# Optimization experiments

Measured on AMD Instinct MI355X. Metric: run time of the kernel, lower is better.

## Reference

```python
import jax, jax.numpy as jnp
import numpy as np

B, S, H = 4, 2048, 512
DEPTH, EXP = 2, 4
MAX_LR = 0.1
C = 8            # n_chunks
L = S // C       # chunk length
HE = H * EXP


def _l2norm(x, eps=1e-12):
    n = jnp.sqrt(jnp.sum(x * x, axis=-1, keepdims=True))
    return x / jnp.maximum(n, eps)


def _mem_fwd(mw1, mb1, mw2, mb2, x):
    # ResLinear: residual MLP blocks, x <- x + W2 @ silu(W1 @ x + b1) + b2
    for d in range(DEPTH):
        h = jax.nn.silu(x @ mw1[d].T + mb1[d])
        x = x + h @ mw2[d].T + mb2[d]
    return x


def setup_inputs() -> dict:
    key = jax.random.key(0)
    ks = jax.random.split(key, 9)
    s = 1.0 / np.sqrt(H)
    s2 = 1.0 / np.sqrt(HE)
    return {
        "x": jax.random.normal(ks[0], (B, S, H), jnp.float32),
        "wq": jax.random.normal(ks[1], (H, H), jnp.float32) * s, "bq": jnp.zeros((H,), jnp.float32),
        "wk": jax.random.normal(ks[2], (H, H), jnp.float32) * s, "bk": jnp.zeros((H,), jnp.float32),
        "wv": jax.random.normal(ks[3], (H, H), jnp.float32) * s, "bv": jnp.zeros((H,), jnp.float32),
        "wlr": jax.random.normal(ks[4], (1, H), jnp.float32) * s, "blr": jnp.zeros((1,), jnp.float32),
        "wf": jax.random.normal(ks[5], (1, H), jnp.float32) * s, "bf": jnp.zeros((1,), jnp.float32),
        "wm": jax.random.normal(ks[6], (1, H), jnp.float32) * s, "bm": jnp.zeros((1,), jnp.float32),
        "mw1": jax.random.normal(ks[7], (DEPTH, HE, H), jnp.float32) * s,
        "mb1": jnp.zeros((DEPTH, HE), jnp.float32),
        "mw2": jax.random.normal(ks[8], (DEPTH, H, HE), jnp.float32) * s2,
        "mb2": jnp.zeros((DEPTH, H), jnp.float32),
        "mom_w1": jnp.zeros((DEPTH, HE, H), jnp.float32),
        "mom_b1": jnp.zeros((DEPTH, HE), jnp.float32),
        "mom_w2": jnp.zeros((DEPTH, H, HE), jnp.float32),
        "mom_b2": jnp.zeros((DEPTH, H), jnp.float32),
    }


def reference(x, wq, bq, wk, bk, wv, bv, wlr, blr, wf, bf, wm, bm,
              mw1, mb1, mw2, mb2, mom_w1, mom_b1, mom_w2, mom_b2):
    # projections (non-generating path; S % C == 0 so no padding)
    q = _l2norm(x @ wq.T + bq)                            # [B,S,H]
    k = _l2norm(x @ wk.T + bk).reshape(B, C, L, H)
    v = (x @ wv.T + bv).reshape(B, C, L, H)
    lr = jax.nn.sigmoid(x @ wlr.T + blr).reshape(B, C, L, 1) * MAX_LR
    forget = jax.nn.sigmoid(x @ wf.T + bf).reshape(B, C, L, 1)
    momg = jax.nn.sigmoid(x @ wm.T + bm).reshape(B, C, L, 1)

    mem = (mw1, mb1, mw2, mb2)

    def chunk_loss(mem_params, k_c, v_c, lr_c):
        # k_c,v_c: [B,L,H]; lr_c: [B,L,1]
        preds = _mem_fwd(*mem_params, k_c)
        loss = jnp.mean((preds - v_c) ** 2, axis=-1)      # [B,L]
        return jnp.sum(loss * lr_c[..., 0])

    # per-chunk synthetic gradients of the memory MLP, then mean over chunks
    grads = jax.vmap(jax.grad(chunk_loss), in_axes=(None, 1, 1, 1))(mem, k, v, lr)
    grads = jax.tree_util.tree_map(lambda g: jnp.mean(g, axis=0), grads)

    alpha = jnp.mean(forget, axis=(1, 2, 3))              # [B] forget gate
    theta = jnp.mean(lr, axis=(1, 2, 3))                  # [B] adaptive lr
    eta = jnp.mean(momg, axis=(1, 2, 3))                  # [B] momentum gate

    def update(p, g, m):
        shp = (B,) + (1,) * p.ndim
        a, t, e = alpha.reshape(shp), theta.reshape(shp), eta.reshape(shp)
        m_b = e * m[None] - t * g[None]                   # [B,*p.shape]
        return jnp.mean(p[None] * (1.0 - a) + m_b, axis=0)

    moms = (mom_w1, mom_b1, mom_w2, mom_b2)
    new_mem = tuple(update(p, g, m) for p, g, m in zip(mem, grads, moms))

    return _mem_fwd(*new_mem, q)                          # [B,S,H]
```

## Files before the change

### kernel.cpp

```cpp
#include <hip/hip_runtime.h>
#include <cstdint>
#include <cstddef>


#define NROWS 8192
#define HDIM  512
#define HEDIM 2048
#define NCHUNK 8
#define BK    64
#define DPCOEF (2.0f / (HDIM * NCHUNK))

typedef unsigned short u16;
typedef __attribute__((ext_vector_type(8))) unsigned short u16x8;
typedef __attribute__((ext_vector_type(8))) short bf16x8;
typedef __attribute__((ext_vector_type(4))) float f32x4;

__device__ __forceinline__ float sigmoidf_(float x){ return 1.0f/(1.0f+__expf(-x)); }
__device__ __forceinline__ float siluf_(float x){ return x*sigmoidf_(x); }
__device__ __forceinline__ float dsiluf_(float x){ float s=sigmoidf_(x); return s*(1.0f+x*(1.0f-s)); }
__device__ __forceinline__ u16 bf1_(float x){
    union{float f; unsigned u;} v; v.f = x;
    return (u16)((v.u + 0x7fffu + ((v.u>>16)&1u)) >> 16);
}
__device__ __forceinline__ unsigned bfpack_(float a, float b){
    union{float f; unsigned u;} ua, ub; ua.f = a; ub.f = b;
    unsigned ra = (ua.u + 0x7fffu + ((ua.u>>16)&1u)) >> 16;
    unsigned rb = (ub.u + 0x7fffu + ((ub.u>>16)&1u)) & 0xffff0000u;
    return ra | rb;
}
__device__ __forceinline__ float bf2f_(u16 h){
    union{unsigned u; float f;} v; v.u = ((unsigned)h) << 16; return v.f;
}
__device__ __forceinline__ int swkey_(int row){
    return (((row>>3)&1)<<2) | (((row>>4)&1)<<1) | ((row>>5)&1);
}
__device__ __forceinline__ void gl_lds16(const u16* g, u16* l){
    __builtin_amdgcn_global_load_lds(
        (const __attribute__((address_space(1))) unsigned*)g,
        (__attribute__((address_space(3))) unsigned*)l, 16, 0, 0);
}
__device__ __forceinline__ void bar_(){ asm volatile("s_barrier" ::: "memory"); }
#define VMCNT8  asm volatile("s_waitcnt vmcnt(8)" ::: "memory")
#define VMCNT0  asm volatile("s_waitcnt vmcnt(0)" ::: "memory")
#define LGKM0   asm volatile("s_waitcnt lgkmcnt(0)" ::: "memory")

template<int MODE, bool ATR>
__global__ __launch_bounds__(256)
void mgemm_k(const u16* __restrict__ A, const u16* __restrict__ B,
             const float* __restrict__ bias, const float* __restrict__ resF,
             const u16* __restrict__ resB, const u16* __restrict__ aux,
             const float* __restrict__ vf, const float* __restrict__ lrs,
             float* __restrict__ outF, u16* __restrict__ outB, u16* __restrict__ outB2,
             int M, int N, int K, int lda, int ldb, int ldv)
{
    constexpr int NBUF = ATR ? 1 : 2;
    __shared__ __align__(128) u16 As[NBUF][128*64];
    __shared__ __align__(128) u16 Bs[NBUF][128*64];
    const int tid = threadIdx.x;
    const int lane = tid & 63, wvi = tid >> 6;
    const int wm = wvi >> 1, wn = wvi & 1;
    const int lr = lane & 15, lq = lane >> 4;

    const int gx = gridDim.x;
    const int nwg = gx * gridDim.y;
    int bid = blockIdx.y * gx + blockIdx.x;
    bid = (bid & 7) * (nwg >> 3) + (bid >> 3);
    const int m0 = (bid / gx) * 128, n0 = (bid % gx) * 128;

    int kbeg = 0, kend = K;
    if (MODE == 3){ const int ks = K >> 4; kbeg = blockIdx.z * ks; kend = kbeg + ks; }
    const int nk = (kend - kbeg) / BK;

    f32x4 acc[4][4];
    const f32x4 zz = {0.f,0.f,0.f,0.f};
    #pragma unroll
    for (int i = 0; i < 4; ++i)
        #pragma unroll
        for (int j = 0; j < 4; ++j) acc[i][j] = zz;

    const int mc = tid & 15, kp = tid >> 4;
    const int tkey = (((mc&1)<<2)|(((mc>>1)&1)<<1)|((mc>>2)&1));
    const int tcs = ((kp >> 1) ^ tkey) * 8 + (kp & 1) * 4;
    u16x8 rgA0, rgA1, rgA2, rgA3, rgB0, rgB1, rgB2, rgB3;

    auto stageNT = [&](int k0, int b){
        #pragma unroll
        for (int it = 0; it < 4; ++it){
            const int seg = it*4 + wvi;
            const int key = (((seg&1)<<2)|(((seg>>1)&1)<<1)|((seg>>2)&1));
            const int row = seg*8 + (lane>>3);
            const int chunk = (lane&7) ^ key;
            gl_lds16(A + (size_t)(m0+row)*lda + k0 + chunk*8, &As[b][seg*512]);
            gl_lds16(B + (size_t)(n0+row)*ldb + k0 + chunk*8, &Bs[b][seg*512]);
        }
    };
    auto gloadTN = [&](int k0){
        const u16* pa = A + (size_t)(k0 + 4*kp) * lda + m0 + mc*8;
        rgA0 = *(const u16x8*)pa;          rgA1 = *(const u16x8*)(pa + lda);
        rgA2 = *(const u16x8*)(pa+2*lda);  rgA3 = *(const u16x8*)(pa + 3*lda);
        const u16* pb = B + (size_t)(k0 + 4*kp) * ldb + n0 + mc*8;
        rgB0 = *(const u16x8*)pb;          rgB1 = *(const u16x8*)(pb + ldb);
        rgB2 = *(const u16x8*)(pb+2*ldb);  rgB3 = *(const u16x8*)(pb + 3*ldb);
    };
    auto dswriteTN = [&](){
        #pragma unroll
        for (int j = 0; j < 8; ++j){
            uint2 w;
            w.x = (unsigned)rgA0[j] | ((unsigned)rgA1[j] << 16);
            w.y = (unsigned)rgA2[j] | ((unsigned)rgA3[j] << 16);
            *(uint2*)&As[0][(mc*8 + j)*64 + tcs] = w;
            uint2 v;
            v.x = (unsigned)rgB0[j] | ((unsigned)rgB1[j] << 16);
            v.y = (unsigned)rgB2[j] | ((unsigned)rgB3[j] << 16);
            *(uint2*)&Bs[0][(mc*8 + j)*64 + tcs] = v;
        }
    };
    auto mfmaStep = [&](int b){
        #pragma unroll
        for (int ks = 0; ks < 2; ++ks) {
            bf16x8 afr[4], bfr[4];
            #pragma unroll
            for (int i = 0; i < 4; ++i){
                const int ra = wm*64 + i*16 + lr, rb = wn*64 + i*16 + lr;
                afr[i] = *(const bf16x8*)&As[b][ra*64 + (((ks*4 + lq) ^ swkey_(ra)) << 3)];
                bfr[i] = *(const bf16x8*)&Bs[b][rb*64 + (((ks*4 + lq) ^ swkey_(rb)) << 3)];
            }
            #pragma unroll
            for (int mi = 0; mi < 4; ++mi)
                #pragma unroll
                for (int ni = 0; ni < 4; ++ni)
                    acc[mi][ni] = __builtin_amdgcn_mfma_f32_16x16x32_bf16(afr[mi], bfr[ni], acc[mi][ni], 0, 0, 0);
        }
    };

    if (!ATR) {
        stageNT(kbeg, 0);
        int cur = 0;
        for (int i = 0; i < nk; ++i){
            const int k0 = kbeg + i*BK;
            if (i + 1 < nk){ stageNT(k0 + BK, cur ^ 1); VMCNT8; }
            else           { VMCNT0; }
            bar_();
            mfmaStep(cur);
            bar_();
            cur ^= 1;
        }
    } else {
        gloadTN(kbeg);
        dswriteTN();
        LGKM0; bar_();
        for (int i = 0; i < nk; ++i){
            const int k0 = kbeg + i*BK;
            const bool hn = (i + 1 < nk);
            if (hn) gloadTN(k0 + BK);
            mfmaStep(0);
            bar_();
            if (hn){ dswriteTN(); LGKM0; }
            bar_();
        }
    }

    if (MODE == 3){
        unsigned* P32 = (unsigned*)outB;
        const size_t zb = (size_t)blockIdx.z * ((size_t)M * N / 2);
        #pragma unroll
        for (int ni = 0; ni < 4; ++ni){
            const int col = n0 + wn*64 + ni*16 + lr;
            #pragma unroll
            for (int mi = 0; mi < 4; ++mi){
                const int pr = (m0 + wm*64 + mi*16 + lq*4) >> 1;
                P32[zb + (size_t)pr*N + col]     = bfpack_(acc[mi][ni][0], acc[mi][ni][1]);
                P32[zb + (size_t)(pr+1)*N + col] = bfpack_(acc[mi][ni][2], acc[mi][ni][3]);
            }
        }
        return;
    }

    #pragma unroll
    for (int ni = 0; ni < 4; ++ni){
        const int col = n0 + wn*64 + ni*16 + lr;
        float bv = 0.0f;
        if (MODE==0 || MODE==1 || MODE==2 || MODE==6 || MODE==7 || MODE==8 || MODE==9) bv = bias[col];
        #pragma unroll
        for (int mi = 0; mi < 4; ++mi){
            const int rbase = m0 + wm*64 + mi*16 + lq*4;
            #pragma unroll
            for (int v = 0; v < 4; ++v){
                const int row = rbase + v;
                const size_t idx = (size_t)row * N + col;
                const float o = acc[mi][ni][v];
                if (MODE == 0){ outF[idx] = o + bv; }
                else if (MODE == 1){
                    const float u = o + bv;
                    outB[idx]  = bf1_(siluf_(u));
                    outB2[idx] = bf1_(dsiluf_(u));
                }
                else if (MODE == 2){ outB[idx] = bf1_(siluf_(o + bv)); }
                else if (MODE == 4){ outB[idx] = bf1_(o * bf2f_(aux[idx])); }
                else if (MODE == 5){ outB[idx] = bf1_(o + resF[idx]); }
                else if (MODE == 6){ const float t = o + bv + resF[idx]; outF[idx] = t; outB[idx] = bf1_(t); }
                else if (MODE == 7){ outF[idx] = o + bv + resF[idx]; }
                else if (MODE == 8){
                    const float t = o + bv + bf2f_(resB[idx]);
                    const float g = lrs[row] * DPCOEF * (t - vf[(size_t)row * ldv + col]);
                    outF[idx] = g; outB[idx] = bf1_(g);
                }
                else if (MODE == 9){ outB[idx] = bf1_(o + bv + bf2f_(resB[idx])); }
            }
        }
    }
}

#define XSLOTS   (NROWS*HDIM/8)
#define KVQSLOTS (3*HDIM*HDIM/8)
__global__ __launch_bounds__(256)
void prep_all_k(const float* __restrict__ x,  u16* __restrict__ xb,
                const float* __restrict__ mw1, u16* __restrict__ mw1b,
                const float* __restrict__ mw2, u16* __restrict__ mw2b,
                const float* __restrict__ wk, const float* __restrict__ wv,
                const float* __restrict__ wq, u16* __restrict__ wkvqb,
                const float* __restrict__ bk, const float* __restrict__ bv,
                const float* __restrict__ bq, float* __restrict__ bkvq)
{
    const int id = blockIdx.x * 256 + threadIdx.x;
    const int W1S = 2*HEDIM*HDIM/8;
    const float* src; u16* dst; int i;
    if (id < XSLOTS){ src = x; dst = xb; i = id; }
    else if (id < XSLOTS + W1S){ src = mw1; dst = mw1b; i = id - XSLOTS; }
    else if (id < XSLOTS + 2*W1S){ src = mw2; dst = mw2b; i = id - XSLOTS - W1S; }
    else if (id < XSLOTS + 2*W1S + KVQSLOTS){
        const int j = id - XSLOTS - 2*W1S;
        const int per = HDIM*HDIM/8;
        src = (j < per) ? wk : (j < 2*per ? wv : wq);
        i = (j < per) ? j : (j < 2*per ? j - per : j - 2*per);
        dst = wkvqb + ((size_t)(j - i)) * 8;
    }
    else {
        const int j = id - XSLOTS - 2*W1S - KVQSLOTS;
        if (j < 3*HDIM)
            bkvq[j] = (j < HDIM) ? bk[j] : (j < 2*HDIM ? bv[j-HDIM] : bq[j-2*HDIM]);
        return;
    }
    const float4 a = *(const float4*)(src + (size_t)i*8);
    const float4 b = *(const float4*)(src + (size_t)i*8 + 4);
    u16x8 o;
    o[0]=bf1_(a.x); o[1]=bf1_(a.y); o[2]=bf1_(a.z); o[3]=bf1_(a.w);
    o[4]=bf1_(b.x); o[5]=bf1_(b.y); o[6]=bf1_(b.z); o[7]=bf1_(b.w);
    *(u16x8*)(dst + (size_t)i*8) = o;
}

__global__ __launch_bounds__(256)
void tcvt_k(const float* __restrict__ in, u16* __restrict__ out, int R, int C)
{
    __shared__ float t[32][33];
    const int tx = threadIdx.x & 31, ty = threadIdx.x >> 5;
    const int c0 = blockIdx.x * 32, r0 = blockIdx.y * 32;
    #pragma unroll
    for (int j = 0; j < 4; ++j)
        t[ty + 8*j][tx] = in[(size_t)(r0 + ty + 8*j) * C + c0 + tx];
    __syncthreads();
    #pragma unroll
    for (int j = 0; j < 4; ++j)
        out[(size_t)(c0 + ty + 8*j) * R + r0 + tx] = bf1_(t[tx][ty + 8*j]);
}

template<bool WF32>
__global__ __launch_bounds__(64)
void l2norm_k(const float* __restrict__ in, int ld,
              float* __restrict__ outF, u16* __restrict__ outB)
{
    const float* p = in + (size_t)blockIdx.x * ld;
    const int t = threadIdx.x;
    float4 v0 = *(const float4*)(p + t*8), v1 = *(const float4*)(p + t*8 + 4);
    float s = v0.x*v0.x+v0.y*v0.y+v0.z*v0.z+v0.w*v0.w
            + v1.x*v1.x+v1.y*v1.y+v1.z*v1.z+v1.w*v1.w;
    #pragma unroll
    for (int o = 1; o < 64; o <<= 1) s += __shfl_xor(s, o);
    const float sc = 1.0f / fmaxf(sqrtf(s), 1e-12f);
    v0.x*=sc; v0.y*=sc; v0.z*=sc; v0.w*=sc;
    v1.x*=sc; v1.y*=sc; v1.z*=sc; v1.w*=sc;
    if (WF32){
        float* q = outF + (size_t)blockIdx.x * HDIM;
        *(float4*)(q + t*8) = v0; *(float4*)(q + t*8 + 4) = v1;
    }
    u16x8 ob;
    ob[0]=bf1_(v0.x); ob[1]=bf1_(v0.y); ob[2]=bf1_(v0.z); ob[3]=bf1_(v0.w);
    ob[4]=bf1_(v1.x); ob[5]=bf1_(v1.y); ob[6]=bf1_(v1.z); ob[7]=bf1_(v1.w);
    *(u16x8*)(outB + (size_t)blockIdx.x * HDIM + t*8) = ob;
}

__global__ __launch_bounds__(64)
void gates_k(const float* __restrict__ x,
             const float* __restrict__ wlr, const float* __restrict__ blr,
             const float* __restrict__ wf,  const float* __restrict__ bfp,
             const float* __restrict__ wm,  const float* __restrict__ bm,
             float* __restrict__ lr_s, float* __restrict__ f_s, float* __restrict__ m_s)
{
    const size_t row = blockIdx.x;
    const float* p = x + row * HDIM;
    const int t = threadIdx.x;
    float s0 = 0.f, s1 = 0.f, s2 = 0.f;
    #pragma unroll
    for (int i = 0; i < 8; i += 4){
        float4 xv = *(const float4*)(p   + t*8 + i);
        float4 a  = *(const float4*)(wlr + t*8 + i);
        float4 b  = *(const float4*)(wf  + t*8 + i);
        float4 c  = *(const float4*)(wm  + t*8 + i);
        s0 += xv.x*a.x + xv.y*a.y + xv.z*a.z + xv.w*a.w;
        s1 += xv.x*b.x + xv.y*b.y + xv.z*b.z + xv.w*b.w;
        s2 += xv.x*c.x + xv.y*c.y + xv.z*c.z + xv.w*c.w;
    }
    #pragma unroll
    for (int o = 1; o < 64; o <<= 1){
        s0 += __shfl_xor(s0, o); s1 += __shfl_xor(s1, o); s2 += __shfl_xor(s2, o);
    }
    if (t == 0){
        lr_s[row] = sigmoidf_(s0 + blr[0]) * 0.1f;
        f_s[row]  = sigmoidf_(s1 + bfp[0]);
        m_s[row]  = sigmoidf_(s2 + bm[0]);
    }
}

__global__ __launch_bounds__(256)
void scalars_k(const float* __restrict__ lr_s, const float* __restrict__ f_s,
               const float* __restrict__ m_s, float* __restrict__ sc)
{
    __shared__ float sh0[256], sh1[256], sh2[256];
    const int t = threadIdx.x;
    float s0 = 0.f, s1 = 0.f, s2 = 0.f;
    for (int i = t; i < NROWS; i += 256){ s0 += f_s[i]; s1 += lr_s[i]; s2 += m_s[i]; }
    sh0[t] = s0; sh1[t] = s1; sh2[t] = s2;
    __syncthreads();
    for (int o = 128; o > 0; o >>= 1){
        if (t < o){ sh0[t] += sh0[t+o]; sh1[t] += sh1[t+o]; sh2[t] += sh2[t+o]; }
        __syncthreads();
    }
    if (t == 0){
        sc[0] = sh0[0] / (float)NROWS;
        sc[1] = sh1[0] / (float)NROWS;
        sc[2] = sh2[0] / (float)NROWS;
    }
}

template<typename T>
__global__ __launch_bounds__(64)
void colsum_part_k(const T* __restrict__ g, float* __restrict__ part, int cols)
{
    const int c = blockIdx.x * 64 + threadIdx.x;
    const int rc = blockIdx.y;
    const T* p = g + (size_t)rc * 128 * cols + c;
    float s = 0.f;
    for (int r = 0; r < 128; ++r){
        if (sizeof(T) == 2) s += bf2f_(*(const u16*)(p + (size_t)r * cols));
        else                s += *(const float*)(p + (size_t)r * cols);
    }
    part[(size_t)rc * cols + c] = s;
}

__global__ __launch_bounds__(256)
void colsum_upd_k(const float* __restrict__ part, const float* __restrict__ p,
                  const float* __restrict__ mom, const float* __restrict__ sc,
                  float* __restrict__ nb, int cols)
{
    const int c = blockIdx.x * 256 + threadIdx.x;
    if (c < cols){
        float s = 0.f;
        for (int r = 0; r < 64; ++r) s += part[(size_t)r * cols + c];
        nb[c] = p[c] * (1.0f - sc[0]) + sc[2] * mom[c] - sc[1] * s;
    }
}

__global__ __launch_bounds__(256)
void fupdate16p_k(const float* __restrict__ p, const unsigned* __restrict__ P32,
                  const float* __restrict__ mom, const float* __restrict__ sc,
                  u16* __restrict__ nWb, int N, int MN2)
{
    const int i = blockIdx.x * 256 + threadIdx.x;
    if (i < MN2){
        float g0 = 0.f, g1 = 0.f;
        #pragma unroll
        for (int z = 0; z < 16; ++z){
            const unsigned w = P32[(size_t)z * MN2 + i];
            g0 += bf2f_((u16)(w & 0xffffu));
            g1 += bf2f_((u16)(w >> 16));
        }
        const int c = i & (N - 1);
        const size_t r0 = ((size_t)(i / N) * 2) * N + c;
        nWb[r0]     = bf1_(p[r0]     * (1.0f - sc[0]) + sc[2] * mom[r0]     - sc[1] * g0);
        nWb[r0 + N] = bf1_(p[r0 + N] * (1.0f - sc[0]) + sc[2] * mom[r0 + N] - sc[1] * g1);
    }
}

extern "C" void kernel_launch(void* const* d_in, const int* in_sizes, int n_in,
                              void* d_out, int out_size, void* d_ws, size_t ws_size,
                              hipStream_t stream)
{
    const float* x      = (const float*)d_in[0];
    const float* wq     = (const float*)d_in[1];
    const float* bq     = (const float*)d_in[2];
    const float* wk     = (const float*)d_in[3];
    const float* bk     = (const float*)d_in[4];
    const float* wv     = (const float*)d_in[5];
    const float* bv     = (const float*)d_in[6];
    const float* wlr    = (const float*)d_in[7];
    const float* blr    = (const float*)d_in[8];
    const float* wf     = (const float*)d_in[9];
    const float* bfp    = (const float*)d_in[10];
    const float* wm     = (const float*)d_in[11];
    const float* bm     = (const float*)d_in[12];
    const float* mw1    = (const float*)d_in[13];
    const float* mb1    = (const float*)d_in[14];
    const float* mw2    = (const float*)d_in[15];
    const float* mb2    = (const float*)d_in[16];
    const float* mom_w1 = (const float*)d_in[17];
    const float* mom_b1 = (const float*)d_in[18];
    const float* mom_w2 = (const float*)d_in[19];
    const float* mom_b2 = (const float*)d_in[20];
    float* out = (float*)d_out;

    char* base = (char*)d_ws;
    size_t off = 0;
    auto alloc = [&](size_t bytes)->char*{ char* p = base + off; off += (bytes + 255) & ~(size_t)255; return p; };
    const size_t NHf  = (size_t)NROWS * HDIM  * 4;
    const size_t NHb  = (size_t)NROWS * HDIM  * 2;
    const size_t NHEb = (size_t)NROWS * HEDIM * 2;
    const int    WHALF = HEDIM * HDIM;

    float* F2   = (float*)alloc(NHf);
    u16*  xb    = (u16*) alloc(NHb);
    u16*  kb    = (u16*) alloc(NHb);
    u16*  x1b   = (u16*) alloc(NHb);
    u16*  g2b   = (u16*) alloc(NHb);
    u16*  hb    = (u16*) alloc(NHEb);
    u16*  db    = (u16*) alloc(NHEb);
    u16*  dhb   = (u16*) alloc(NHEb + NHf);
    u16*  wkvqb = (u16*) alloc((size_t)3*HDIM*HDIM*2);
    float* bkvq = (float*)alloc((size_t)3*HDIM*4);
    u16*  mw1b  = (u16*) alloc((size_t)2*WHALF*2);
    u16*  mw2b  = (u16*) alloc((size_t)2*WHALF*2);
    u16*  mw2Tb = (u16*) alloc((size_t)2*WHALF*2);
    u16*  mw1T1b= (u16*) alloc((size_t)WHALF*2);
    u16*  nW1b  = (u16*) alloc((size_t)2*WHALF*2);
    u16*  nW2b  = (u16*) alloc((size_t)2*WHALF*2);
    float* cpart= (float*)alloc((size_t)64*HEDIM*4);
    float* lr_s = (float*)alloc((size_t)NROWS*4);
    float* f_s  = (float*)alloc((size_t)NROWS*4);
    float* m_s  = (float*)alloc((size_t)NROWS*4);
    float* sc   = (float*)alloc(64);
    float* nb1  = (float*)alloc((size_t)2*HEDIM*4);
    float* nb2  = (float*)alloc((size_t)2*HDIM*4);

    const bool keep0 = (ws_size >= off + 2*NHEb + 1024);
    u16* h0b = keep0 ? (u16*)alloc(NHEb) : hb;
    u16* d0b = keep0 ? (u16*)alloc(NHEb) : db;

    u16* qb  = xb;
    u16* g1b = g2b;
    float* P3 = (float*)dhb;
    float* F1 = (float*)((char*)dhb + NHEb);
    unsigned* Pp = (unsigned*)db;

    const dim3 blk(256);
    const dim3 gKVQ (3*HDIM/128, NROWS/128);
    const dim3 gN512 (HDIM/128,  NROWS/128);
    const dim3 gN2048(HEDIM/128, NROWS/128);
    const dim3 gTN2  (HEDIM/128, HDIM/128, 16);
    const dim3 gTN1  (HDIM/128,  HEDIM/128, 16);
    const int MN2 = WHALF / 2;

    const float* mw1_1 = mw1 + (size_t)WHALF;
    const float* mw2_1 = mw2 + (size_t)WHALF;

    #define GARG(Ab,Bb,bi,rF,rB,ax,vv,ll,oF,oB,oB2,M,N,K,la,lb,lv) \
        ((const u16*)(Ab),(const u16*)(Bb),(const float*)(bi),(const float*)(rF),\
         (const u16*)(rB),(const u16*)(ax),(const float*)(vv),(const float*)(ll),\
         (float*)(oF),(u16*)(oB),(u16*)(oB2),(M),(N),(K),(la),(lb),(lv))

    {
        const int nblk = (XSLOTS + 2*(2*HEDIM*HDIM/8) + KVQSLOTS)/256 + (3*HDIM + 255)/256;
        prep_all_k<<<dim3(nblk), blk, 0, stream>>>(x, xb, mw1, mw1b, mw2, mw2b,
                                                   wk, wv, wq, wkvqb, bk, bv, bq, bkvq);
    }
    tcvt_k<<<dim3(HEDIM/32, HDIM/32), blk, 0, stream>>>(mw2,   mw2Tb,         HDIM, HEDIM);
    tcvt_k<<<dim3(HEDIM/32, HDIM/32), blk, 0, stream>>>(mw2_1, mw2Tb + WHALF, HDIM, HEDIM);
    tcvt_k<<<dim3(HDIM/32, HEDIM/32), blk, 0, stream>>>(mw1_1, mw1T1b,        HEDIM, HDIM);
    gates_k<<<NROWS, 64, 0, stream>>>(x, wlr, blr, wf, bfp, wm, bm, lr_s, f_s, m_s);
    scalars_k<<<1, blk, 0, stream>>>(lr_s, f_s, m_s, sc);

    mgemm_k<0,false><<<gKVQ, blk, 0, stream>>>GARG(xb, wkvqb, bkvq, 0,0,0,0,0, P3, 0,0, NROWS,3*HDIM,HDIM, HDIM,HDIM, 3*HDIM);
    l2norm_k<false><<<NROWS, 64, 0, stream>>>(P3,          3*HDIM, nullptr, kb);
    l2norm_k<true ><<<NROWS, 64, 0, stream>>>(P3 + 2*HDIM, 3*HDIM, F2, qb);

    if (keep0)
        mgemm_k<1,false><<<gN2048, blk, 0, stream>>>GARG(kb, mw1b, mb1, 0,0,0,0,0, 0, h0b, d0b, NROWS,HEDIM,HDIM, HDIM,HDIM, HEDIM);
    else
        mgemm_k<2,false><<<gN2048, blk, 0, stream>>>GARG(kb, mw1b, mb1, 0,0,0,0,0, 0, hb, 0, NROWS,HEDIM,HDIM, HDIM,HDIM, HEDIM);
    mgemm_k<9,false><<<gN512, blk, 0, stream>>>GARG(h0b, mw2b, mb2, 0, kb, 0,0,0, 0, x1b, 0, NROWS,HDIM,HEDIM, HEDIM,HEDIM, HDIM);
    mgemm_k<1,false><<<gN2048, blk, 0, stream>>>GARG(x1b, mw1b+WHALF, mb1+HEDIM, 0,0,0,0,0, 0, hb, db, NROWS,HEDIM,HDIM, HDIM,HDIM, HEDIM);
    mgemm_k<8,false><<<gN512, blk, 0, stream>>>GARG(hb, mw2b+WHALF, mb2+HDIM, 0, x1b, 0, P3 + HDIM, lr_s, out, g2b, 0, NROWS,HDIM,HEDIM, HEDIM,HEDIM, 3*HDIM);

    colsum_part_k<float><<<dim3(HDIM/64,64), 64, 0, stream>>>(out, cpart, HDIM);
    colsum_upd_k<<<dim3(HDIM/256), blk, 0, stream>>>(cpart, mb2+HDIM, mom_b2+HDIM, sc, nb2+HDIM, HDIM);
    mgemm_k<4,false><<<gN2048, blk, 0, stream>>>GARG(g2b, mw2Tb+WHALF, 0,0,0, db, 0,0, 0, dhb, 0, NROWS,HEDIM,HDIM, HDIM,HDIM, HEDIM);
    mgemm_k<3,true><<<gTN2, blk, 0, stream>>>GARG(g2b, hb, 0,0,0,0,0,0, 0, Pp, 0, HDIM,HEDIM,NROWS, HDIM,HEDIM, HEDIM);
    fupdate16p_k<<<dim3((MN2+255)/256), blk, 0, stream>>>(mw2_1, Pp, mom_w2+WHALF, sc, nW2b+WHALF, HEDIM, MN2);
    colsum_part_k<u16><<<dim3(HEDIM/64,64), 64, 0, stream>>>(dhb, cpart, HEDIM);
    colsum_upd_k<<<dim3(HEDIM/256), blk, 0, stream>>>(cpart, mb1+HEDIM, mom_b1+HEDIM, sc, nb1+HEDIM, HEDIM);
    mgemm_k<3,true><<<gTN1, blk, 0, stream>>>GARG(dhb, x1b, 0,0,0,0,0,0, 0, Pp, 0, HEDIM,HDIM,NROWS, HEDIM,HDIM, HDIM);
    fupdate16p_k<<<dim3((MN2+255)/256), blk, 0, stream>>>(mw1_1, Pp, mom_w1+WHALF, sc, nW1b+WHALF, HDIM, MN2);
    mgemm_k<5,false><<<gN512, blk, 0, stream>>>GARG(dhb, mw1T1b, 0, out, 0,0,0,0, 0, g1b, 0, NROWS,HDIM,HEDIM, HEDIM,HEDIM, HDIM);

    colsum_part_k<u16><<<dim3(HDIM/64,64), 64, 0, stream>>>(g1b, cpart, HDIM);
    colsum_upd_k<<<dim3(HDIM/256), blk, 0, stream>>>(cpart, mb2, mom_b2, sc, nb2, HDIM);
    if (!keep0)
        mgemm_k<1,false><<<gN2048, blk, 0, stream>>>GARG(kb, mw1b, mb1, 0,0,0,0,0, 0, hb, db, NROWS,HEDIM,HDIM, HDIM,HDIM, HEDIM);
    mgemm_k<4,false><<<gN2048, blk, 0, stream>>>GARG(g1b, mw2Tb, 0,0,0, d0b, 0,0, 0, dhb, 0, NROWS,HEDIM,HDIM, HDIM,HDIM, HEDIM);
    mgemm_k<3,true><<<gTN2, blk, 0, stream>>>GARG(g1b, h0b, 0,0,0,0,0,0, 0, Pp, 0, HDIM,HEDIM,NROWS, HDIM,HEDIM, HEDIM);
    fupdate16p_k<<<dim3((MN2+255)/256), blk, 0, stream>>>(mw2, Pp, mom_w2, sc, nW2b, HEDIM, MN2);
    colsum_part_k<u16><<<dim3(HEDIM/64,64), 64, 0, stream>>>(dhb, cpart, HEDIM);
    colsum_upd_k<<<dim3(HEDIM/256), blk, 0, stream>>>(cpart, mb1, mom_b1, sc, nb1, HEDIM);
    mgemm_k<3,true><<<gTN1, blk, 0, stream>>>GARG(dhb, kb, 0,0,0,0,0,0, 0, Pp, 0, HEDIM,HDIM,NROWS, HEDIM,HDIM, HDIM);
    fupdate16p_k<<<dim3((MN2+255)/256), blk, 0, stream>>>(mw1, Pp, mom_w1, sc, nW1b, HDIM, MN2);

    mgemm_k<2,false><<<gN2048, blk, 0, stream>>>GARG(qb, nW1b, nb1, 0,0,0,0,0, 0, hb, 0, NROWS,HEDIM,HDIM, HDIM,HDIM, HEDIM);
    mgemm_k<6,false><<<gN512, blk, 0, stream>>>GARG(hb, nW2b, nb2, F2, 0,0,0,0, F1, x1b, 0, NROWS,HDIM,HEDIM, HEDIM,HEDIM, HDIM);
    mgemm_k<2,false><<<gN2048, blk, 0, stream>>>GARG(x1b, nW1b+WHALF, nb1+HEDIM, 0,0,0,0,0, 0, hb, 0, NROWS,HEDIM,HDIM, HDIM,HDIM, HEDIM);
    mgemm_k<7,false><<<gN512, blk, 0, stream>>>GARG(hb, nW2b+WHALF, nb2+HDIM, F1, 0,0,0,0, out, 0,0, NROWS,HDIM,HEDIM, HEDIM,HEDIM, HDIM);

    #undef GARG
    (void)in_sizes; (void)n_in; (void)out_size;
}
```

Before: 790.4 us.

## Fuse column-sum reductions into GEMM epilogues and store intermediates in bf16

Column sums for the bias gradients are now reduced inside the GEMM epilogue through an LDS reduction that writes per-128-row partials. This removes the separate colsum_part kernels and their re-reads of the gradient matrices. The KVQ projection now writes bf16 instead of fp32, l2norm reads bf16, and the MODE 8 epilogue stops writing an fp32 gradient copy, which cuts memory traffic. The keep0 path that cached first-layer activations is dropped, so the layer-0 forward GEMM is always recomputed later, and storing intermediates in bf16 costs some precision.

```diff
diff --git a/kernel.cpp b/kernel.cpp
--- a/kernel.cpp
+++ b/kernel.cpp
@@ -44,13 +44,14 @@
 #define VMCNT0  asm volatile("s_waitcnt vmcnt(0)" ::: "memory")
 #define LGKM0   asm volatile("s_waitcnt lgkmcnt(0)" ::: "memory")
 
-template<int MODE, bool ATR>
+template<int MODE, bool ATR, bool CSUM>
 __global__ __launch_bounds__(256)
 void mgemm_k(const u16* __restrict__ A, const u16* __restrict__ B,
              const float* __restrict__ bias, const float* __restrict__ resF,
              const u16* __restrict__ resB, const u16* __restrict__ aux,
-             const float* __restrict__ vf, const float* __restrict__ lrs,
+             const float* __restrict__ lrs,
              float* __restrict__ outF, u16* __restrict__ outB, u16* __restrict__ outB2,
+             float* __restrict__ cpart,
              int M, int N, int K, int lda, int ldb, int ldv)
 {
     constexpr int NBUF = ATR ? 1 : 2;
@@ -148,15 +149,16 @@
     } else {
         gloadTN(kbeg);
         dswriteTN();
-        LGKM0; bar_();
+        LGKM0;
+        __syncthreads();
         for (int i = 0; i < nk; ++i){
             const int k0 = kbeg + i*BK;
             const bool hn = (i + 1 < nk);
             if (hn) gloadTN(k0 + BK);
             mfmaStep(0);
-            bar_();
+            __syncthreads();
             if (hn){ dswriteTN(); LGKM0; }
-            bar_();
+            __syncthreads();
         }
     }
 
@@ -176,11 +178,12 @@
         return;
     }
 
+    float cs[4] = {0.f, 0.f, 0.f, 0.f};
     #pragma unroll
     for (int ni = 0; ni < 4; ++ni){
         const int col = n0 + wn*64 + ni*16 + lr;
         float bv = 0.0f;
-        if (MODE==0 || MODE==1 || MODE==2 || MODE==6 || MODE==7 || MODE==8 || MODE==9) bv = bias[col];
+        if (MODE==1 || MODE==2 || MODE==6 || MODE==7 || MODE==8 || MODE==9 || MODE==10) bv = bias[col];
         #pragma unroll
         for (int mi = 0; mi < 4; ++mi){
             const int rbase = m0 + wm*64 + mi*16 + lq*4;
@@ -189,24 +192,47 @@
                 const int row = rbase + v;
                 const size_t idx = (size_t)row * N + col;
                 const float o = acc[mi][ni][v];
-                if (MODE == 0){ outF[idx] = o + bv; }
-                else if (MODE == 1){
+                if (MODE == 1){
                     const float u = o + bv;
                     outB[idx]  = bf1_(siluf_(u));
                     outB2[idx] = bf1_(dsiluf_(u));
                 }
                 else if (MODE == 2){ outB[idx] = bf1_(siluf_(o + bv)); }
-                else if (MODE == 4){ outB[idx] = bf1_(o * bf2f_(aux[idx])); }
-                else if (MODE == 5){ outB[idx] = bf1_(o + resF[idx]); }
+                else if (MODE == 4){
+                    const float t = o * bf2f_(aux[idx]);
+                    outB[idx] = bf1_(t);
+                    if (CSUM) cs[ni] += t;
+                }
+                else if (MODE == 5){
+                    const float t = o + bf2f_(resB[idx]);
+                    outB[idx] = bf1_(t);
+                    if (CSUM) cs[ni] += t;
+                }
                 else if (MODE == 6){ const float t = o + bv + resF[idx]; outF[idx] = t; outB[idx] = bf1_(t); }
                 else if (MODE == 7){ outF[idx] = o + bv + resF[idx]; }
                 else if (MODE == 8){
                     const float t = o + bv + bf2f_(resB[idx]);
-                    const float g = lrs[row] * DPCOEF * (t - vf[(size_t)row * ldv + col]);
-                    outF[idx] = g; outB[idx] = bf1_(g);
+                    const float g = lrs[row] * DPCOEF * (t - bf2f_(aux[(size_t)row * ldv + col]));
+                    outB[idx] = bf1_(g);
+                    if (CSUM) cs[ni] += g;
                 }
                 else if (MODE == 9){ outB[idx] = bf1_(o + bv + bf2f_(resB[idx])); }
+                else if (MODE == 10){ outB[idx] = bf1_(o + bv); }
             }
+        }
+    }
+
+    if (CSUM){
+        float* red = (float*)&As[0][0];
+        #pragma unroll
+        for (int ni = 0; ni < 4; ++ni)
+            red[(wm*4 + lq)*128 + wn*64 + ni*16 + lr] = cs[ni];
+        __syncthreads();
+        if (tid < 128){
+            float s = 0.f;
+            #pragma unroll
+            for (int z = 0; z < 8; ++z) s += red[z*128 + tid];
+            cpart[(size_t)(m0 >> 7) * N + n0 + tid] = s;
         }
     }
 }
@@ -266,26 +292,31 @@
 
 template<bool WF32>
 __global__ __launch_bounds__(64)
-void l2norm_k(const float* __restrict__ in, int ld,
+void l2norm_k(const u16* __restrict__ in, int ld,
               float* __restrict__ outF, u16* __restrict__ outB)
 {
-    const float* p = in + (size_t)blockIdx.x * ld;
+    const u16* p = in + (size_t)blockIdx.x * ld;
     const int t = threadIdx.x;
-    float4 v0 = *(const float4*)(p + t*8), v1 = *(const float4*)(p + t*8 + 4);
-    float s = v0.x*v0.x+v0.y*v0.y+v0.z*v0.z+v0.w*v0.w
-            + v1.x*v1.x+v1.y*v1.y+v1.z*v1.z+v1.w*v1.w;
+    u16x8 v = *(const u16x8*)(p + t*8);
+    float f[8];
+    #pragma unroll
+    for (int j = 0; j < 8; ++j) f[j] = bf2f_(v[j]);
+    float s = 0.f;
+    #pragma unroll
+    for (int j = 0; j < 8; ++j) s += f[j]*f[j];
     #pragma unroll
     for (int o = 1; o < 64; o <<= 1) s += __shfl_xor(s, o);
     const float sc = 1.0f / fmaxf(sqrtf(s), 1e-12f);
-    v0.x*=sc; v0.y*=sc; v0.z*=sc; v0.w*=sc;
-    v1.x*=sc; v1.y*=sc; v1.z*=sc; v1.w*=sc;
+    #pragma unroll
+    for (int j = 0; j < 8; ++j) f[j] *= sc;
     if (WF32){
-        float* q = outF + (size_t)blockIdx.x * HDIM;
-        *(float4*)(q + t*8) = v0; *(float4*)(q + t*8 + 4) = v1;
+        float* q = outF + (size_t)blockIdx.x * HDIM + t*8;
+        *(float4*)q     = make_float4(f[0], f[1], f[2], f[3]);
+        *(float4*)(q+4) = make_float4(f[4], f[5], f[6], f[7]);
     }
     u16x8 ob;
-    ob[0]=bf1_(v0.x); ob[1]=bf1_(v0.y); ob[2]=bf1_(v0.z); ob[3]=bf1_(v0.w);
-    ob[4]=bf1_(v1.x); ob[5]=bf1_(v1.y); ob[6]=bf1_(v1.z); ob[7]=bf1_(v1.w);
+    #pragma unroll
+    for (int j = 0; j < 8; ++j) ob[j] = bf1_(f[j]);
     *(u16x8*)(outB + (size_t)blockIdx.x * HDIM + t*8) = ob;
 }
 
@@ -340,21 +371,6 @@
         sc[1] = sh1[0] / (float)NROWS;
         sc[2] = sh2[0] / (float)NROWS;
     }
-}
-
-template<typename T>
-__global__ __launch_bounds__(64)
-void colsum_part_k(const T* __restrict__ g, float* __restrict__ part, int cols)
-{
-    const int c = blockIdx.x * 64 + threadIdx.x;
-    const int rc = blockIdx.y;
-    const T* p = g + (size_t)rc * 128 * cols + c;
-    float s = 0.f;
-    for (int r = 0; r < 128; ++r){
-        if (sizeof(T) == 2) s += bf2f_(*(const u16*)(p + (size_t)r * cols));
-        else                s += *(const float*)(p + (size_t)r * cols);
-    }
-    part[(size_t)rc * cols + c] = s;
 }
 
 __global__ __launch_bounds__(256)
@@ -450,13 +466,9 @@
     float* nb1  = (float*)alloc((size_t)2*HEDIM*4);
     float* nb2  = (float*)alloc((size_t)2*HDIM*4);
 
-    const bool keep0 = (ws_size >= off + 2*NHEb + 1024);
-    u16* h0b = keep0 ? (u16*)alloc(NHEb) : hb;
-    u16* d0b = keep0 ? (u16*)alloc(NHEb) : db;
-
     u16* qb  = xb;
     u16* g1b = g2b;
-    float* P3 = (float*)dhb;
+    u16* P3b = dhb;
     float* F1 = (float*)((char*)dhb + NHEb);
     unsigned* Pp = (unsigned*)db;
 
@@ -471,10 +483,10 @@
     const float* mw1_1 = mw1 + (size_t)WHALF;
     const float* mw2_1 = mw2 + (size_t)WHALF;
 
-    #define GARG(Ab,Bb,bi,rF,rB,ax,vv,ll,oF,oB,oB2,M,N,K,la,lb,lv) \
+    #define GARG(Ab,Bb,bi,rF,rB,ax,ll,oF,oB,oB2,cp,M,N,K,la,lb,lv) \
         ((const u16*)(Ab),(const u16*)(Bb),(const float*)(bi),(const float*)(rF),\
-         (const u16*)(rB),(const u16*)(ax),(const float*)(vv),(const float*)(ll),\
-         (float*)(oF),(u16*)(oB),(u16*)(oB2),(M),(N),(K),(la),(lb),(lv))
+         (const u16*)(rB),(const u16*)(ax),(const float*)(ll),\
+         (float*)(oF),(u16*)(oB),(u16*)(oB2),(float*)(cp),(M),(N),(K),(la),(lb),(lv))
 
     {
         const int nblk = (XSLOTS + 2*(2*HEDIM*HDIM/8) + KVQSLOTS)/256 + (3*HDIM + 255)/256;
@@ -487,46 +499,38 @@
     gates_k<<<NROWS, 64, 0, stream>>>(x, wlr, blr, wf, bfp, wm, bm, lr_s, f_s, m_s);
     scalars_k<<<1, blk, 0, stream>>>(lr_s, f_s, m_s, sc);
 
-    mgemm_k<0,false><<<gKVQ, blk, 0, stream>>>GARG(xb, wkvqb, bkvq, 0,0,0,0,0, P3, 0,0, NROWS,3*HDIM,HDIM, HDIM,HDIM, 3*HDIM);
-    l2norm_k<false><<<NROWS, 64, 0, stream>>>(P3,          3*HDIM, nullptr, kb);
-    l2norm_k<true ><<<NROWS, 64, 0, stream>>>(P3 + 2*HDIM, 3*HDIM, F2, qb);
-
-    if (keep0)
-        mgemm_k<1,false><<<gN2048, blk, 0, stream>>>GARG(kb, mw1b, mb1, 0,0,0,0,0, 0, h0b, d0b, NROWS,HEDIM,HDIM, HDIM,HDIM, HEDIM);
-    else
-        mgemm_k<2,false><<<gN2048, blk, 0, stream>>>GARG(kb, mw1b, mb1, 0,0,0,0,0, 0, hb, 0, NROWS,HEDIM,HDIM, HDIM,HDIM, HEDIM);
-    mgemm_k<9,false><<<gN512, blk, 0, stream>>>GARG(h0b, mw2b, mb2, 0, kb, 0,0,0, 0, x1b, 0, NROWS,HDIM,HEDIM, HEDIM,HEDIM, HDIM);
-    mgemm_k<1,false><<<gN2048, blk, 0, stream>>>GARG(x1b, mw1b+WHALF, mb1+HEDIM, 0,0,0,0,0, 0, hb, db, NROWS,HEDIM,HDIM, HDIM,HDIM, HEDIM);
-    mgemm_k<8,false><<<gN512, blk, 0, stream>>>GARG(hb, mw2b+WHALF, mb2+HDIM, 0, x1b, 0, P3 + HDIM, lr_s, out, g2b, 0, NROWS,HDIM,HEDIM, HEDIM,HEDIM, 3*HDIM);
-
-    colsum_part_k<float><<<dim3(HDIM/64,64), 64, 0, stream>>>(out, cpart, HDIM);
+    mgemm_k<10,false,false><<<gKVQ, blk, 0, stream>>>GARG(xb, wkvqb, bkvq, 0,0,0,0, 0, P3b, 0, 0, NROWS,3*HDIM,HDIM, HDIM,HDIM, 0);
+    l2norm_k<false><<<NROWS, 64, 0, stream>>>(P3b,          3*HDIM, nullptr, kb);
+    l2norm_k<true ><<<NROWS, 64, 0, stream>>>(P3b + 2*HDIM, 3*HDIM, F2, qb);
+
+    mgemm_k<2,false,false><<<gN2048, blk, 0, stream>>>GARG(kb, mw1b, mb1, 0,0,0,0, 0, hb, 0, 0, NROWS,HEDIM,HDIM, HDIM,HDIM, 0);
+    mgemm_k<9,false,false><<<gN512, blk, 0, stream>>>GARG(hb, mw2b, mb2, 0, kb, 0,0, 0, x1b, 0, 0, NROWS,HDIM,HEDIM, HEDIM,HEDIM, 0);
+    mgemm_k<1,false,false><<<gN2048, blk, 0, stream>>>GARG(x1b, mw1b+WHALF, mb1+HEDIM, 0,0,0,0, 0, hb, db, 0, NROWS,HEDIM,HDIM, HDIM,HDIM, 0);
+    mgemm_k<8,false,true><<<gN512, blk, 0, stream>>>GARG(hb, mw2b+WHALF, mb2+HDIM, 0, x1b, P3b + HDIM, lr_s, 0, g2b, 0, cpart, NROWS,HDIM,HEDIM, HEDIM,HEDIM, 3*HDIM);
+
     colsum_upd_k<<<dim3(HDIM/256), blk, 0, stream>>>(cpart, mb2+HDIM, mom_b2+HDIM, sc, nb2+HDIM, HDIM);
-    mgemm_k<4,false><<<gN2048, blk, 0, stream>>>GARG(g2b, mw2Tb+WHALF, 0,0,0, db, 0,0, 0, dhb, 0, NROWS,HEDIM,HDIM, HDIM,HDIM, HEDIM);
-    mgemm_k<3,true><<<gTN2, blk, 0, stream>>>GARG(g2b, hb, 0,0,0,0,0,0, 0, Pp, 0, HDIM,HEDIM,NROWS, HDIM,HEDIM, HEDIM);
+    mgemm_k<4,false,true><<<gN2048, blk, 0, stream>>>GARG(g2b, mw2Tb+WHALF, 0,0,0, db, 0, 0, dhb, 0, cpart, NROWS,HEDIM,HDIM, HDIM,HDIM, 0);
+    mgemm_k<3,true,false><<<gTN2, blk, 0, stream>>>GARG(g2b, hb, 0,0,0,0,0, 0, Pp, 0, 0, HDIM,HEDIM,NROWS, HDIM,HEDIM, 0);
     fupdate16p_k<<<dim3((MN2+255)/256), blk, 0, stream>>>(mw2_1, Pp, mom_w2+WHALF, sc, nW2b+WHALF, HEDIM, MN2);
-    colsum_part_k<u16><<<dim3(HEDIM/64,64), 64, 0, stream>>>(dhb, cpart, HEDIM);
     colsum_upd_k<<<dim3(HEDIM/256), blk, 0, stream>>>(cpart, mb1+HEDIM, mom_b1+HEDIM, sc, nb1+HEDIM, HEDIM);
-    mgemm_k<3,true><<<gTN1, blk, 0, stream>>>GARG(dhb, x1b, 0,0,0,0,0,0, 0, Pp, 0, HEDIM,HDIM,NROWS, HEDIM,HDIM, HDIM);
+    mgemm_k<3,true,false><<<gTN1, blk, 0, stream>>>GARG(dhb, x1b, 0,0,0,0,0, 0, Pp, 0, 0, HEDIM,HDIM,NROWS, HEDIM,HDIM, 0);
     fupdate16p_k<<<dim3((MN2+255)/256), blk, 0, stream>>>(mw1_1, Pp, mom_w1+WHALF, sc, nW1b+WHALF, HDIM, MN2);
-    mgemm_k<5,false><<<gN512, blk, 0, stream>>>GARG(dhb, mw1T1b, 0, out, 0,0,0,0, 0, g1b, 0, NROWS,HDIM,HEDIM, HEDIM,HEDIM, HDIM);
-
-    colsum_part_k<u16><<<dim3(HDIM/64,64), 64, 0, stream>>>(g1b, cpart, HDIM);
+    mgemm_k<5,false,true><<<gN512, blk, 0, stream>>>GARG(dhb, mw1T1b, 0, 0, g2b, 0, 0, 0, g1b, 0, cpart, NROWS,HDIM,HEDIM, HEDIM,HEDIM, 0);
+
     colsum_upd_k<<<dim3(HDIM/256), blk, 0, stream>>>(cpart, mb2, mom_b2, sc, nb2, HDIM);
-    if (!keep0)
-        mgemm_k<1,false><<<gN2048, blk, 0, stream>>>GARG(kb, mw1b, mb1, 0,0,0,0,0, 0, hb, db, NROWS,HEDIM,HDIM, HDIM,HDIM, HEDIM);
-    mgemm_k<4,false><<<gN2048, blk, 0, stream>>>GARG(g1b, mw2Tb, 0,0,0, d0b, 0,0, 0, dhb, 0, NROWS,HEDIM,HDIM, HDIM,HDIM, HEDIM);
-    mgemm_k<3,true><<<gTN2, blk, 0, stream>>>GARG(g1b, h0b, 0,0,0,0,0,0, 0, Pp, 0, HDIM,HEDIM,NROWS, HDIM,HEDIM, HEDIM);
+    mgemm_k<1,false,false><<<gN2048, blk, 0, stream>>>GARG(kb, mw1b, mb1, 0,0,0,0, 0, hb, db, 0, NROWS,HEDIM,HDIM, HDIM,HDIM, 0);
+    mgemm_k<4,false,true><<<gN2048, blk, 0, stream>>>GARG(g1b, mw2Tb, 0,0,0, db, 0, 0, dhb, 0, cpart, NROWS,HEDIM,HDIM, HDIM,HDIM, 0);
+    mgemm_k<3,true,false><<<gTN2, blk, 0, stream>>>GARG(g1b, hb, 0,0,0,0,0, 0, Pp, 0, 0, HDIM,HEDIM,NROWS, HDIM,HEDIM, 0);
     fupdate16p_k<<<dim3((MN2+255)/256), blk, 0, stream>>>(mw2, Pp, mom_w2, sc, nW2b, HEDIM, MN2);
-    colsum_part_k<u16><<<dim3(HEDIM/64,64), 64, 0, stream>>>(dhb, cpart, HEDIM);
     colsum_upd_k<<<dim3(HEDIM/256), blk, 0, stream>>>(cpart, mb1, mom_b1, sc, nb1, HEDIM);
-    mgemm_k<3,true><<<gTN1, blk, 0, stream>>>GARG(dhb, kb, 0,0,0,0,0,0, 0, Pp, 0, HEDIM,HDIM,NROWS, HEDIM,HDIM, HDIM);
+    mgemm_k<3,true,false><<<gTN1, blk, 0, stream>>>GARG(dhb, kb, 0,0,0,0,0, 0, Pp, 0, 0, HEDIM,HDIM,NROWS, HEDIM,HDIM, 0);
     fupdate16p_k<<<dim3((MN2+255)/256), blk, 0, stream>>>(mw1, Pp, mom_w1, sc, nW1b, HDIM, MN2);
 
-    mgemm_k<2,false><<<gN2048, blk, 0, stream>>>GARG(qb, nW1b, nb1, 0,0,0,0,0, 0, hb, 0, NROWS,HEDIM,HDIM, HDIM,HDIM, HEDIM);
-    mgemm_k<6,false><<<gN512, blk, 0, stream>>>GARG(hb, nW2b, nb2, F2, 0,0,0,0, F1, x1b, 0, NROWS,HDIM,HEDIM, HEDIM,HEDIM, HDIM);
-    mgemm_k<2,false><<<gN2048, blk, 0, stream>>>GARG(x1b, nW1b+WHALF, nb1+HEDIM, 0,0,0,0,0, 0, hb, 0, NROWS,HEDIM,HDIM, HDIM,HDIM, HEDIM);
-    mgemm_k<7,false><<<gN512, blk, 0, stream>>>GARG(hb, nW2b+WHALF, nb2+HDIM, F1, 0,0,0,0, out, 0,0, NROWS,HDIM,HEDIM, HEDIM,HEDIM, HDIM);
+    mgemm_k<2,false,false><<<gN2048, blk, 0, stream>>>GARG(qb, nW1b, nb1, 0,0,0,0, 0, hb, 0, 0, NROWS,HEDIM,HDIM, HDIM,HDIM, 0);
+    mgemm_k<6,false,false><<<gN512, blk, 0, stream>>>GARG(hb, nW2b, nb2, F2, 0,0,0, F1, x1b, 0, 0, NROWS,HDIM,HEDIM, HEDIM,HEDIM, 0);
+    mgemm_k<2,false,false><<<gN2048, blk, 0, stream>>>GARG(x1b, nW1b+WHALF, nb1+HEDIM, 0,0,0,0, 0, hb, 0, 0, NROWS,HEDIM,HDIM, HDIM,HDIM, 0);
+    mgemm_k<7,false,false><<<gN512, blk, 0, stream>>>GARG(hb, nW2b+WHALF, nb2+HDIM, F1, 0,0,0, out, 0, 0, 0, NROWS,HDIM,HEDIM, HEDIM,HEDIM, 0);
 
     #undef GARG
-    (void)in_sizes; (void)n_in; (void)out_size;
-}
+    (void)in_sizes; (void)n_in; (void)out_size; (void)ws_size;
+}
```

Result: faster. 700.0 us (-11.4%).
